# Kernel optimization log

Measured on AMD Instinct MI355X. Metric: run time of the kernel, lower is better.

The kernel has to match this reference:

```python
import jax, jax.numpy as jnp
import numpy as np

N_NODES = 100000   # embedding table rows
FEAT = 512         # feat_dim F
BATCH = 8192       # seed nodes per batch
DEG = 32           # sampled neighbors per node (col 0 = self)
BN_EPS = 1e-5


def setup_inputs() -> dict:
    key = jax.random.key(0)
    ks = jax.random.split(key, 6)
    feat_table = jax.random.normal(ks[0], (N_NODES, FEAT), dtype=jnp.float32)
    W_gen = jax.random.normal(ks[1], (2 * FEAT, 2 * FEAT), dtype=jnp.float32) * 0.02
    weight1 = jax.random.normal(ks[2], (3 * FEAT, 3 * FEAT), dtype=jnp.float32) * 0.02
    gamma = jnp.ones((3 * FEAT,), dtype=jnp.float32)
    beta = jnp.zeros((3 * FEAT,), dtype=jnp.float32)
    nodes = jax.random.randint(ks[3], (BATCH,), 0, N_NODES, dtype=jnp.int32)
    neigh_idx = jax.random.randint(ks[4], (BATCH, DEG), 0, N_NODES, dtype=jnp.int32)
    neigh_idx = neigh_idx.at[:, 0].set(nodes)  # self node included, as in samp_neighs
    return {"feat_table": feat_table, "W_gen": W_gen, "weight1": weight1,
            "gamma": gamma, "beta": beta, "nodes": nodes, "neigh_idx": neigh_idx}


def _batchnorm_train(x, gamma, beta):
    # BatchNorm1d in training mode: biased batch statistics over axis 0
    mu = x.mean(axis=0)
    var = x.var(axis=0)
    return (x - mu) * jax.lax.rsqrt(var + BN_EPS) * gamma + beta


def _gen(x, W_gen):
    # generator module: raw = x @ W_gen, gen = relu(raw) (shape-preserving [B,2F])
    raw = x @ W_gen
    return jax.nn.relu(raw), raw


def reference(feat_table, W_gen, weight1, gamma, beta, nodes, neigh_idx):
    # self features: [B, F]
    self_feats = feat_table[nodes]
    # gather neighbor feats [B, K, F] and mean-pool (replaces dense mask.mm)
    neigh_feats = feat_table[neigh_idx]
    agg_feats = neigh_feats.mean(axis=1)                 # [B, F]
    cat_feats = jnp.concatenate([self_feats, agg_feats], axis=1)  # [B, 2F]
    gen_feats, raw_feats = _gen(cat_feats, W_gen)        # [B, 2F] each

    # environment aggregation: self node (column 0) removed from neighbor set
    env_agg_feats = neigh_feats[:, 1:, :].mean(axis=1)   # [B, F]
    env_cat = jnp.concatenate([jnp.zeros_like(self_feats), env_agg_feats], axis=1)
    env_gen_feats, env_raw_feats = _gen(env_cat, W_gen)

    # train_flag=True, rl_train_flag=False path
    feats = jnp.concatenate([agg_feats, gen_feats], axis=1)  # [B, 3F]
    to_feats = jax.nn.relu(_batchnorm_train(feats, gamma, beta) @ weight1)
    return (agg_feats, to_feats, gen_feats, raw_feats, env_gen_feats, env_raw_feats)
```

## Files before the change

### kernel.cpp

```cpp
#include <hip/hip_runtime.h>
#include <hip/hip_bf16.h>

typedef unsigned short u16;
typedef unsigned int u32;
typedef __attribute__((ext_vector_type(8))) short short8;
typedef __attribute__((ext_vector_type(4))) float f32x4;

#define BATCH 8192
#define FEAT 512
#define DEG 32
#define BM 128
#define BN 128
#define BK 32
#define LDS_STRIDE 40

__device__ __forceinline__ float b2f(u16 h){
  union { u32 u; float f; } x; x.u = ((u32)h) << 16; return x.f;
}
__device__ __forceinline__ u16 f2b(float f){
  __hip_bfloat16 h = __float2bfloat16(f);
  return *reinterpret_cast<u16*>(&h);
}
__device__ __forceinline__ u32 pack2(float lo, float hi){
  return (u32)f2b(lo) | (((u32)f2b(hi)) << 16);
}

__device__ __forceinline__ f32x4 mfma_bf16_16x16x32(short8 a, short8 b, f32x4 c){
  asm("v_mfma_f32_16x16x32_bf16 %0, %1, %2, %0" : "+v"(c) : "v"(a), "v"(b));
  return c;
}

__global__ __launch_bounds__(256) void gather_agg(
    const float* __restrict__ feat, const int* __restrict__ nodes,
    const int* __restrict__ nidx, float* __restrict__ out_agg,
    u16* __restrict__ cat_bf)
{
  const int b = blockIdx.x;
  const int t = threadIdx.x;
  __shared__ int idx[DEG];
  __shared__ int self_node;
  if (t < DEG) idx[t] = nidx[b * DEG + t];
  if (t == 64) self_node = nodes[b];
  __syncthreads();
  const int f = t * 2;
  float s0 = 0.f, s1 = 0.f;
  #pragma unroll 8
  for (int k = 0; k < DEG; ++k){
    const float2 v = *(const float2*)(feat + (size_t)idx[k] * FEAT + f);
    s0 += v.x; s1 += v.y;
  }
  const float2 sv = *(const float2*)(feat + (size_t)self_node * FEAT + f);
  const float a0 = s0 * (1.f/32.f), a1 = s1 * (1.f/32.f);
  *(float2*)(out_agg + (size_t)b * FEAT + f) = make_float2(a0, a1);
  *(u32*)(cat_bf + (size_t)b * 1024 + f) = pack2(sv.x, sv.y);
  *(u32*)(cat_bf + (size_t)b * 1024 + FEAT + f) = pack2(a0, a1);
}

__global__ __launch_bounds__(256) void transpose_f2b(
    const float* __restrict__ in, u16* __restrict__ out, int R, int C)
{
  __shared__ float tile[32][33];
  const int c0 = blockIdx.x * 32, r0 = blockIdx.y * 32;
  const int x = threadIdx.x, y = threadIdx.y;
  #pragma unroll
  for (int i = 0; i < 32; i += 8)
    tile[y + i][x] = in[(size_t)(r0 + y + i) * C + (c0 + x)];
  __syncthreads();
  #pragma unroll
  for (int i = 0; i < 32; i += 8)
    out[(size_t)(c0 + y + i) * R + (r0 + x)] = f2b(tile[x][y + i]);
}

template<int MODE>
__global__ __launch_bounds__(256) void gemm_bt(
    const u16* __restrict__ A1, const float* __restrict__ A2f,
    const float* __restrict__ sArr, const float* __restrict__ tArr,
    const u16* __restrict__ BT, int ldb, int K,
    float* __restrict__ Craw, float* __restrict__ Crelu, int ldc)
{
  __shared__ __align__(16) u16 As[BM * LDS_STRIDE];
  __shared__ __align__(16) u16 Bs[BN * LDS_STRIDE];
  const int m0 = blockIdx.y * BM;
  const int n0 = blockIdx.x * BN;
  const int t = threadIdx.x;
  const int wave = t >> 6, lane = t & 63;
  const int wr = wave >> 1, wc = wave & 1;
  const int lm = lane & 15, quad = lane >> 4;

  f32x4 acc[4][4] = {};

  const int arow = t >> 1;
  const int aseg = (t & 1) * 16;
  const int m = m0 + arow;

  for (int k0 = 0; k0 < K; k0 += BK){
    const int kk = k0 + aseg;
    u16 buf[16];
    if (MODE == 0){
      const u16* src = A1 + (size_t)m * 1024 + kk;
      *(uint4*)buf = *(const uint4*)src;
      *(uint4*)(buf + 8) = *(const uint4*)(src + 8);
    } else if (MODE == 1){
      const u16* ap = A1 + (size_t)m * 1024 + 512 + kk;
      const u16* sp = A1 + (size_t)m * 1024 + kk;
      u16 ab[16], sb[16];
      *(uint4*)ab = *(const uint4*)ap; *(uint4*)(ab + 8) = *(const uint4*)(ap + 8);
      *(uint4*)sb = *(const uint4*)sp; *(uint4*)(sb + 8) = *(const uint4*)(sp + 8);
      #pragma unroll
      for (int j = 0; j < 16; ++j)
        buf[j] = f2b((32.f * b2f(ab[j]) - b2f(sb[j])) * (1.f/31.f));
    } else {
      float xs[16];
      if (kk < 512){
        const u16* src = A1 + (size_t)m * 1024 + 512 + kk;
        u16 tmp[16];
        *(uint4*)tmp = *(const uint4*)src; *(uint4*)(tmp + 8) = *(const uint4*)(src + 8);
        #pragma unroll
        for (int j = 0; j < 16; ++j) xs[j] = b2f(tmp[j]);
      } else {
        const float4* s4 = (const float4*)(A2f + (size_t)m * 1024 + (kk - 512));
        *(float4*)(xs)      = s4[0];
        *(float4*)(xs + 4)  = s4[1];
        *(float4*)(xs + 8)  = s4[2];
        *(float4*)(xs + 12) = s4[3];
      }
      #pragma unroll
      for (int j = 0; j < 16; ++j)
        buf[j] = f2b(fmaf(xs[j], sArr[kk + j], tArr[kk + j]));
    }
    *(uint4*)&As[arow * LDS_STRIDE + aseg] = *(uint4*)buf;
    *(uint4*)&As[arow * LDS_STRIDE + aseg + 8] = *(uint4*)(buf + 8);
    {
      const uint4* src = (const uint4*)(BT + (size_t)(n0 + arow) * ldb + kk);
      uint4 v0 = src[0], v1 = src[1];
      *(uint4*)&Bs[arow * LDS_STRIDE + aseg] = v0;
      *(uint4*)&Bs[arow * LDS_STRIDE + aseg + 8] = v1;
    }
    __syncthreads();
    short8 af[4], bf[4];
    #pragma unroll
    for (int i = 0; i < 4; ++i)
      af[i] = *(const short8*)&As[(wr * 64 + i * 16 + lm) * LDS_STRIDE + quad * 8];
    #pragma unroll
    for (int j = 0; j < 4; ++j)
      bf[j] = *(const short8*)&Bs[(wc * 64 + j * 16 + lm) * LDS_STRIDE + quad * 8];
    #pragma unroll
    for (int i = 0; i < 4; ++i)
      #pragma unroll
      for (int j = 0; j < 4; ++j)
        acc[i][j] = mfma_bf16_16x16x32(af[i], bf[j], acc[i][j]);
    __syncthreads();
  }
  #pragma unroll
  for (int i = 0; i < 4; ++i){
    const int row = m0 + wr * 64 + i * 16 + quad * 4;
    #pragma unroll
    for (int j = 0; j < 4; ++j){
      const int col = n0 + wc * 64 + j * 16 + lm;
      #pragma unroll
      for (int r = 0; r < 4; ++r){
        const float v = acc[i][j][r];
        const size_t off = (size_t)(row + r) * ldc + col;
        if (MODE != 2){
          Craw[off]  = v;
          Crelu[off] = fmaxf(v, 0.f);
        } else {
          Crelu[off] = fmaxf(v, 0.f);
        }
      }
    }
  }
}

__global__ __launch_bounds__(256) void zero_f32(float* __restrict__ p, int n){
  const int i = blockIdx.x * 256 + threadIdx.x;
  if (i < n) p[i] = 0.f;
}

__global__ __launch_bounds__(256) void bn_partial(
    const u16* __restrict__ cat_bf, const float* __restrict__ gen,
    float* __restrict__ sums)
{
  const int l = threadIdx.x & 63;
  const int ty = threadIdx.x >> 6;
  const int c = blockIdx.x * 64 + l;
  const int r0 = blockIdx.y * 1024;
  float s = 0.f, q = 0.f;
  if (c < 512){
    for (int r = r0 + ty; r < r0 + 1024; r += 4){
      const float x = b2f(cat_bf[(size_t)r * 1024 + 512 + c]);
      s += x; q += x * x;
    }
  } else {
    for (int r = r0 + ty; r < r0 + 1024; r += 4){
      const float x = gen[(size_t)r * 1024 + (c - 512)];
      s += x; q += x * x;
    }
  }
  __shared__ float sh[2][4][64];
  sh[0][ty][l] = s; sh[1][ty][l] = q;
  __syncthreads();
  if (ty == 0){
    s = sh[0][0][l] + sh[0][1][l] + sh[0][2][l] + sh[0][3][l];
    q = sh[1][0][l] + sh[1][1][l] + sh[1][2][l] + sh[1][3][l];
    atomicAdd(&sums[c], s);
    atomicAdd(&sums[1536 + c], q);
  }
}

__global__ __launch_bounds__(256) void bn_finalize(
    const float* __restrict__ sums, const float* __restrict__ gamma,
    const float* __restrict__ beta, float* __restrict__ sArr, float* __restrict__ tArr)
{
  const int c = blockIdx.x * 256 + threadIdx.x;
  if (c >= 1536) return;
  const float mean = sums[c] * (1.f / 8192.f);
  const float var = sums[1536 + c] * (1.f / 8192.f) - mean * mean;
  const float rs = rsqrtf(var + 1e-5f);
  const float sc = gamma[c] * rs;
  sArr[c] = sc;
  tArr[c] = beta[c] - mean * sc;
}

extern "C" void kernel_launch(void* const* d_in, const int* in_sizes, int n_in,
                              void* d_out, int out_size, void* d_ws, size_t ws_size,
                              hipStream_t stream)
{
  const float* feat  = (const float*)d_in[0];
  const float* Wgen  = (const float*)d_in[1];
  const float* W1    = (const float*)d_in[2];
  const float* gamma = (const float*)d_in[3];
  const float* beta  = (const float*)d_in[4];
  const int* nodes   = (const int*)d_in[5];
  const int* nidx    = (const int*)d_in[6];

  float* o = (float*)d_out;
  float* out_agg    = o;
  float* out_to     = o + 4194304;
  float* out_gen    = o + 16777216;
  float* out_raw    = o + 25165824;
  float* out_envgen = o + 33554432;
  float* out_envraw = o + 41943040;

  char* w = (char*)d_ws;
  float* sums = (float*)w;
  float* sArr = (float*)(w + 12288);
  float* tArr = (float*)(w + 18432);
  u16* wgT    = (u16*)(w + 32768);
  u16* w1T    = (u16*)(w + 2129920);
  u16* cat_bf = (u16*)(w + 6848512);

  gather_agg<<<BATCH, 256, 0, stream>>>(feat, nodes, nidx, out_agg, cat_bf);
  transpose_f2b<<<dim3(32, 32), dim3(32, 8), 0, stream>>>(Wgen, wgT, 1024, 1024);
  transpose_f2b<<<dim3(48, 48), dim3(32, 8), 0, stream>>>(W1, w1T, 1536, 1536);

  gemm_bt<0><<<dim3(8, 64), 256, 0, stream>>>(
      cat_bf, nullptr, nullptr, nullptr, wgT, 1024, 1024,
      out_raw, out_gen, 1024);
  gemm_bt<1><<<dim3(8, 64), 256, 0, stream>>>(
      cat_bf, nullptr, nullptr, nullptr, wgT + 512, 1024, 512,
      out_envraw, out_envgen, 1024);

  zero_f32<<<12, 256, 0, stream>>>(sums, 3072);
  bn_partial<<<dim3(24, 8), 256, 0, stream>>>(cat_bf, out_gen, sums);
  bn_finalize<<<6, 256, 0, stream>>>(sums, gamma, beta, sArr, tArr);

  gemm_bt<2><<<dim3(12, 64), 256, 0, stream>>>(
      cat_bf, out_gen, sArr, tArr, w1T, 1536, 1536,
      nullptr, out_to, 1536);
}
```

Before: 638.5 us.

## Precompute bf16 GEMM operands and load tiles via global_load_lds

The GEMM A-operand preprocessing (env mean derivation, batchnorm affine plus bf16 cast) moves out of the GEMM inner loops. The env mean is now computed in the gather kernel and batchnorm is applied in a new prep kernel that writes a bf16 matrix. The GEMM tile loads now use direct global-to-LDS loads with an unpadded 32-element stride, and the two generator GEMMs are merged into one launch via grid z. This adds extra passes over global memory and unpadded LDS rows that may cause bank conflicts, in exchange for simpler and faster GEMM main loops.

```diff
diff --git a/kernel.cpp b/kernel.cpp
--- a/kernel.cpp
+++ b/kernel.cpp
@@ -12,7 +12,6 @@
 #define BM 128
 #define BN 128
 #define BK 32
-#define LDS_STRIDE 40
 
 __device__ __forceinline__ float b2f(u16 h){
   union { u32 u; float f; } x; x.u = ((u32)h) << 16; return x.f;
@@ -30,10 +29,16 @@
   return c;
 }
 
+__device__ __forceinline__ void gload16(const u16* g, u16* l){
+  __builtin_amdgcn_global_load_lds(
+      (const __attribute__((address_space(1))) u32*)(const void*)g,
+      (__attribute__((address_space(3))) u32*)(void*)l, 16, 0, 0);
+}
+
 __global__ __launch_bounds__(256) void gather_agg(
     const float* __restrict__ feat, const int* __restrict__ nodes,
     const int* __restrict__ nidx, float* __restrict__ out_agg,
-    u16* __restrict__ cat_bf)
+    u16* __restrict__ cat_bf, u16* __restrict__ env_bf)
 {
   const int b = blockIdx.x;
   const int t = threadIdx.x;
@@ -51,9 +56,11 @@
   }
   const float2 sv = *(const float2*)(feat + (size_t)self_node * FEAT + f);
   const float a0 = s0 * (1.f/32.f), a1 = s1 * (1.f/32.f);
+  const float e0 = (s0 - sv.x) * (1.f/31.f), e1 = (s1 - sv.y) * (1.f/31.f);
   *(float2*)(out_agg + (size_t)b * FEAT + f) = make_float2(a0, a1);
   *(u32*)(cat_bf + (size_t)b * 1024 + f) = pack2(sv.x, sv.y);
   *(u32*)(cat_bf + (size_t)b * 1024 + FEAT + f) = pack2(a0, a1);
+  *(u32*)(env_bf + (size_t)b * FEAT + f) = pack2(e0, e1);
 }
 
 __global__ __launch_bounds__(256) void transpose_f2b(
@@ -71,79 +78,35 @@
     out[(size_t)(c0 + y + i) * R + (r0 + x)] = f2b(tile[x][y + i]);
 }
 
-template<int MODE>
-__global__ __launch_bounds__(256) void gemm_bt(
-    const u16* __restrict__ A1, const float* __restrict__ A2f,
-    const float* __restrict__ sArr, const float* __restrict__ tArr,
-    const u16* __restrict__ BT, int ldb, int K,
-    float* __restrict__ Craw, float* __restrict__ Crelu, int ldc)
-{
-  __shared__ __align__(16) u16 As[BM * LDS_STRIDE];
-  __shared__ __align__(16) u16 Bs[BN * LDS_STRIDE];
-  const int m0 = blockIdx.y * BM;
-  const int n0 = blockIdx.x * BN;
+template<bool WRITE_RAW>
+__device__ __forceinline__ void gemm_body(
+    const u16* __restrict__ A, int lda, const u16* __restrict__ BT, int ldb,
+    int K, float* __restrict__ Craw, float* __restrict__ Crelu, int ldc,
+    int m0, int n0, u16* As, u16* Bs)
+{
   const int t = threadIdx.x;
   const int wave = t >> 6, lane = t & 63;
   const int wr = wave >> 1, wc = wave & 1;
   const int lm = lane & 15, quad = lane >> 4;
 
+  const int sr = wave * 32 + (lane >> 2);
+  const int sc = (lane & 3) * 8;
+
   f32x4 acc[4][4] = {};
 
-  const int arow = t >> 1;
-  const int aseg = (t & 1) * 16;
-  const int m = m0 + arow;
-
   for (int k0 = 0; k0 < K; k0 += BK){
-    const int kk = k0 + aseg;
-    u16 buf[16];
-    if (MODE == 0){
-      const u16* src = A1 + (size_t)m * 1024 + kk;
-      *(uint4*)buf = *(const uint4*)src;
-      *(uint4*)(buf + 8) = *(const uint4*)(src + 8);
-    } else if (MODE == 1){
-      const u16* ap = A1 + (size_t)m * 1024 + 512 + kk;
-      const u16* sp = A1 + (size_t)m * 1024 + kk;
-      u16 ab[16], sb[16];
-      *(uint4*)ab = *(const uint4*)ap; *(uint4*)(ab + 8) = *(const uint4*)(ap + 8);
-      *(uint4*)sb = *(const uint4*)sp; *(uint4*)(sb + 8) = *(const uint4*)(sp + 8);
-      #pragma unroll
-      for (int j = 0; j < 16; ++j)
-        buf[j] = f2b((32.f * b2f(ab[j]) - b2f(sb[j])) * (1.f/31.f));
-    } else {
-      float xs[16];
-      if (kk < 512){
-        const u16* src = A1 + (size_t)m * 1024 + 512 + kk;
-        u16 tmp[16];
-        *(uint4*)tmp = *(const uint4*)src; *(uint4*)(tmp + 8) = *(const uint4*)(src + 8);
-        #pragma unroll
-        for (int j = 0; j < 16; ++j) xs[j] = b2f(tmp[j]);
-      } else {
-        const float4* s4 = (const float4*)(A2f + (size_t)m * 1024 + (kk - 512));
-        *(float4*)(xs)      = s4[0];
-        *(float4*)(xs + 4)  = s4[1];
-        *(float4*)(xs + 8)  = s4[2];
-        *(float4*)(xs + 12) = s4[3];
-      }
-      #pragma unroll
-      for (int j = 0; j < 16; ++j)
-        buf[j] = f2b(fmaf(xs[j], sArr[kk + j], tArr[kk + j]));
-    }
-    *(uint4*)&As[arow * LDS_STRIDE + aseg] = *(uint4*)buf;
-    *(uint4*)&As[arow * LDS_STRIDE + aseg + 8] = *(uint4*)(buf + 8);
-    {
-      const uint4* src = (const uint4*)(BT + (size_t)(n0 + arow) * ldb + kk);
-      uint4 v0 = src[0], v1 = src[1];
-      *(uint4*)&Bs[arow * LDS_STRIDE + aseg] = v0;
-      *(uint4*)&Bs[arow * LDS_STRIDE + aseg + 8] = v1;
-    }
+    gload16(A  + (size_t)(m0 + sr)      * lda + k0 + sc, As + sr * 32 + sc);
+    gload16(A  + (size_t)(m0 + sr + 16) * lda + k0 + sc, As + (sr + 16) * 32 + sc);
+    gload16(BT + (size_t)(n0 + sr)      * ldb + k0 + sc, Bs + sr * 32 + sc);
+    gload16(BT + (size_t)(n0 + sr + 16) * ldb + k0 + sc, Bs + (sr + 16) * 32 + sc);
     __syncthreads();
     short8 af[4], bf[4];
     #pragma unroll
     for (int i = 0; i < 4; ++i)
-      af[i] = *(const short8*)&As[(wr * 64 + i * 16 + lm) * LDS_STRIDE + quad * 8];
+      af[i] = *(const short8*)&As[(wr * 64 + i * 16 + lm) * 32 + quad * 8];
     #pragma unroll
     for (int j = 0; j < 4; ++j)
-      bf[j] = *(const short8*)&Bs[(wc * 64 + j * 16 + lm) * LDS_STRIDE + quad * 8];
+      bf[j] = *(const short8*)&Bs[(wc * 64 + j * 16 + lm) * 32 + quad * 8];
     #pragma unroll
     for (int i = 0; i < 4; ++i)
       #pragma unroll
@@ -161,15 +124,40 @@
       for (int r = 0; r < 4; ++r){
         const float v = acc[i][j][r];
         const size_t off = (size_t)(row + r) * ldc + col;
-        if (MODE != 2){
-          Craw[off]  = v;
-          Crelu[off] = fmaxf(v, 0.f);
-        } else {
-          Crelu[off] = fmaxf(v, 0.f);
-        }
+        if (WRITE_RAW) Craw[off] = v;
+        Crelu[off] = fmaxf(v, 0.f);
       }
     }
   }
+}
+
+__global__ __launch_bounds__(256) void gemm12(
+    const u16* __restrict__ catA, const u16* __restrict__ envA,
+    const u16* __restrict__ wgT,
+    float* __restrict__ raw, float* __restrict__ gen,
+    float* __restrict__ envraw, float* __restrict__ envgen)
+{
+  __shared__ __align__(16) u16 As[BM * BK];
+  __shared__ __align__(16) u16 Bs[BN * BK];
+  const int z = blockIdx.z;
+  const u16* A  = z ? envA : catA;
+  const int lda = z ? 512 : 1024;
+  const int K   = z ? 512 : 1024;
+  const u16* BT = z ? wgT + 512 : wgT;
+  float* Craw   = z ? envraw : raw;
+  float* Crelu  = z ? envgen : gen;
+  gemm_body<true>(A, lda, BT, 1024, K, Craw, Crelu, 1024,
+                  blockIdx.y * BM, blockIdx.x * BN, As, Bs);
+}
+
+__global__ __launch_bounds__(256) void gemm3(
+    const u16* __restrict__ bnA, const u16* __restrict__ w1T,
+    float* __restrict__ to_out)
+{
+  __shared__ __align__(16) u16 As[BM * BK];
+  __shared__ __align__(16) u16 Bs[BN * BK];
+  gemm_body<false>(bnA, 1536, w1T, 1536, 1536, nullptr, to_out, 1536,
+                   blockIdx.y * BM, blockIdx.x * BN, As, Bs);
 }
 
 __global__ __launch_bounds__(256) void zero_f32(float* __restrict__ p, int n){
@@ -178,7 +166,7 @@
 }
 
 __global__ __launch_bounds__(256) void bn_partial(
-    const u16* __restrict__ cat_bf, const float* __restrict__ gen,
+    const float* __restrict__ agg, const float* __restrict__ gen,
     float* __restrict__ sums)
 {
   const int l = threadIdx.x & 63;
@@ -188,7 +176,7 @@
   float s = 0.f, q = 0.f;
   if (c < 512){
     for (int r = r0 + ty; r < r0 + 1024; r += 4){
-      const float x = b2f(cat_bf[(size_t)r * 1024 + 512 + c]);
+      const float x = agg[(size_t)r * 512 + c];
       s += x; q += x * x;
     }
   } else {
@@ -222,6 +210,24 @@
   tArr[c] = beta[c] - mean * sc;
 }
 
+__global__ __launch_bounds__(384) void prep_bnA(
+    const float* __restrict__ agg, const float* __restrict__ gen,
+    const float* __restrict__ sArr, const float* __restrict__ tArr,
+    u16* __restrict__ bnA)
+{
+  const int m = blockIdx.x;
+  const int t = threadIdx.x;
+  const int c = t * 4;
+  const float4 x = (c < 512)
+      ? *(const float4*)(agg + (size_t)m * 512 + c)
+      : *(const float4*)(gen + (size_t)m * 1024 + (c - 512));
+  const float4 s4 = *(const float4*)(sArr + c);
+  const float4 t4 = *(const float4*)(tArr + c);
+  const u32 lo = pack2(fmaf(x.x, s4.x, t4.x), fmaf(x.y, s4.y, t4.y));
+  const u32 hi = pack2(fmaf(x.z, s4.z, t4.z), fmaf(x.w, s4.w, t4.w));
+  *(uint2*)(bnA + (size_t)m * 1536 + c) = make_uint2(lo, hi);
+}
+
 extern "C" void kernel_launch(void* const* d_in, const int* in_sizes, int n_in,
                               void* d_out, int out_size, void* d_ws, size_t ws_size,
                               hipStream_t stream)
@@ -249,23 +255,20 @@
   u16* wgT    = (u16*)(w + 32768);
   u16* w1T    = (u16*)(w + 2129920);
   u16* cat_bf = (u16*)(w + 6848512);
-
-  gather_agg<<<BATCH, 256, 0, stream>>>(feat, nodes, nidx, out_agg, cat_bf);
+  u16* env_bf = (u16*)(w + 23625728);
+  u16* bnA_bf = (u16*)(w + 6848512);
+
+  gather_agg<<<BATCH, 256, 0, stream>>>(feat, nodes, nidx, out_agg, cat_bf, env_bf);
   transpose_f2b<<<dim3(32, 32), dim3(32, 8), 0, stream>>>(Wgen, wgT, 1024, 1024);
   transpose_f2b<<<dim3(48, 48), dim3(32, 8), 0, stream>>>(W1, w1T, 1536, 1536);
 
-  gemm_bt<0><<<dim3(8, 64), 256, 0, stream>>>(
-      cat_bf, nullptr, nullptr, nullptr, wgT, 1024, 1024,
-      out_raw, out_gen, 1024);
-  gemm_bt<1><<<dim3(8, 64), 256, 0, stream>>>(
-      cat_bf, nullptr, nullptr, nullptr, wgT + 512, 1024, 512,
-      out_envraw, out_envgen, 1024);
+  gemm12<<<dim3(8, 64, 2), 256, 0, stream>>>(
+      cat_bf, env_bf, wgT, out_raw, out_gen, out_envraw, out_envgen);
 
   zero_f32<<<12, 256, 0, stream>>>(sums, 3072);
-  bn_partial<<<dim3(24, 8), 256, 0, stream>>>(cat_bf, out_gen, sums);
+  bn_partial<<<dim3(24, 8), 256, 0, stream>>>(out_agg, out_gen, sums);
   bn_finalize<<<6, 256, 0, stream>>>(sums, gamma, beta, sArr, tArr);
-
-  gemm_bt<2><<<dim3(12, 64), 256, 0, stream>>>(
-      cat_bf, out_gen, sArr, tArr, w1T, 1536, 1536,
-      nullptr, out_to, 1536);
-}
+  prep_bnA<<<BATCH, 384, 0, stream>>>(out_agg, out_gen, sArr, tArr, bnA_bf);
+
+  gemm3<<<dim3(12, 64), 256, 0, stream>>>(bnA_bf, w1T, out_to);
+}
```

Result: faster. 598.9 us (-6.2%).
